# Optimization experiments

Measured on AMD Instinct MI355X. Metric: run time of the kernel, lower is better.

## Reference

```python
import jax, jax.numpy as jnp
import numpy as np

WINDOW = 512  # sliding-window size (keys per query, including self)


def setup_inputs() -> dict:
    key = jax.random.key(0)
    ks = jax.random.split(key, 5)
    B, T, C = 2, 8192, 1024
    s = 1.0 / np.sqrt(C)
    return {
        "x": jax.random.normal(ks[0], (B, T, C), dtype=jnp.float32),
        "Wq": jax.random.normal(ks[1], (C, C), dtype=jnp.float32) * s,
        "Wk": jax.random.normal(ks[2], (C, C), dtype=jnp.float32) * s,
        "Wv": jax.random.normal(ks[3], (C, C), dtype=jnp.float32) * s,
        "Wo": jax.random.normal(ks[4], (C, C), dtype=jnp.float32) * s,
    }


def _block_local_attn(q, k, v, window):
    # q,k,v: [B,H,T,D]; causal sliding-window attention, honoring sparsity by
    # attending only to the current and previous block of size `window`.
    B, H, T, D = q.shape
    W = window
    nb = T // W
    scale = 1.0 / jnp.sqrt(jnp.asarray(D, q.dtype))
    qb = q.reshape(B, H, nb, W, D)
    kb = k.reshape(B, H, nb, W, D)
    vb = v.reshape(B, H, nb, W, D)
    # previous block (zero-padded for block 0)
    kp = jnp.pad(kb, ((0, 0), (0, 0), (1, 0), (0, 0), (0, 0)))[:, :, :nb]
    vp = jnp.pad(vb, ((0, 0), (0, 0), (1, 0), (0, 0), (0, 0)))[:, :, :nb]
    k2 = jnp.concatenate([kp, kb], axis=3)  # [B,H,nb,2W,D]
    v2 = jnp.concatenate([vp, vb], axis=3)
    i = jnp.arange(W)[:, None]          # query index within block
    j = jnp.arange(2 * W)[None, :]      # key index (0..W-1 prev, W..2W-1 cur)
    # key global offset = j - W relative to query block start; causal window of
    # size W (self + W-1 previous) <=> i < j <= i + W
    base = (j > i) & (j <= i + W)                                  # [W,2W]
    prev_ok = (jnp.arange(nb)[:, None] > 0) | (jnp.arange(2 * W)[None, :] >= W)
    mask = base[None, :, :] & prev_ok[:, None, :]                  # [nb,W,2W]
    scores = jnp.einsum("bhnqd,bhnkd->bhnqk", qb, k2) * scale
    scores = jnp.where(mask[None, None], scores, jnp.asarray(-1e30, scores.dtype))
    p = jax.nn.softmax(scores, axis=-1)
    out = jnp.einsum("bhnqk,bhnkd->bhnqd", p, v2)
    return out.reshape(B, H, T, D)


def reference(x, Wq, Wk, Wv, Wo):
    B, T, C = x.shape
    H = 16
    D = C // H
    # nn.Linear(y = x @ W^T), bias=False
    q = (x @ Wq.T).reshape(B, T, H, D).transpose(0, 2, 1, 3)
    k = (x @ Wk.T).reshape(B, T, H, D).transpose(0, 2, 1, 3)
    v = (x @ Wv.T).reshape(B, T, H, D).transpose(0, 2, 1, 3)
    out = _block_local_attn(q, k, v, WINDOW)
    out = out.transpose(0, 2, 1, 3).reshape(B, T, C)
    return out @ Wo.T
```

## Files before the change

kernel.cpp:

```cpp
#include <hip/hip_runtime.h>
#include <hip/hip_bf16.h>
#include <stdint.h>

typedef __attribute__((ext_vector_type(8))) short short8;
typedef __attribute__((ext_vector_type(4))) float f32x4;
typedef __hip_bfloat16 bf16;

#define AS1 __attribute__((address_space(1)))
#define AS3 __attribute__((address_space(3)))

__device__ __forceinline__ void gl16(const void* g, void* l) {
  __builtin_amdgcn_global_load_lds((const AS1 unsigned int*)g,
                                   (AS3 unsigned int*)l, 16, 0, 0);
}

__device__ __forceinline__ unsigned short bfbits(float x) {
  union { bf16 b; unsigned short u; } c; c.b = __float2bfloat16(x); return c.u;
}

#define SCHED0 __builtin_amdgcn_sched_barrier(0)

__global__ __launch_bounds__(256) void k_cvt(const float* __restrict__ src,
                                             bf16* __restrict__ dst, int n8) {
  int i = blockIdx.x * blockDim.x + threadIdx.x;
  int stride = gridDim.x * blockDim.x;
  for (; i < n8; i += stride) {
    const float4* p = (const float4*)src + (size_t)i * 2;
    float4 a = p[0], b = p[1];
    bf16 tmp[8];
    tmp[0] = __float2bfloat16(a.x); tmp[1] = __float2bfloat16(a.y);
    tmp[2] = __float2bfloat16(a.z); tmp[3] = __float2bfloat16(a.w);
    tmp[4] = __float2bfloat16(b.x); tmp[5] = __float2bfloat16(b.y);
    tmp[6] = __float2bfloat16(b.z); tmp[7] = __float2bfloat16(b.w);
    *(short8*)(dst + (size_t)i * 8) = *(short8*)tmp;
  }
}


#define GEMM_BODY(...)                                                         \
  const int Kd = 1024;                                                         \
  const int nk = 32;                                              \
  __shared__ bf16 As[4][256 * 32];                                             \
  __shared__ bf16 Bs[4][256 * 32];                                             \
  int tid = threadIdx.x;                                                       \
  int lane = tid & 63, wid = tid >> 6;                                         \
  int l15 = lane & 15, hi = lane >> 4;                                         \
  int wm = wid >> 2, wn = wid & 3;                                             \
  f32x4 acc[8][4];                                                             \
  _Pragma("unroll") for (int i = 0; i < 8; i++)                                \
      _Pragma("unroll") for (int j = 0; j < 4; j++)                            \
          acc[i][j] = (f32x4){0.f, 0.f, 0.f, 0.f};                             \
  auto stageA = [&](int slot, int kk) {                                        \
    const bf16* ab = Abase + kk * 32;                                          \
    _Pragma("unroll") for (int pass = 0; pass < 2; pass++) {                   \
      int p = pass * 512 + tid;                                                \
      int row = p >> 2;                                                        \
      int u = (p & 3) ^ ((row >> 1) & 3);                                      \
      gl16(ab + (size_t)row * Kd + u * 8, (char*)(&As[slot][0]) + p * 16);     \
    }                                                                          \
  };                                                                           \
  auto stageB = [&](int slot, int kk) {                                        \
    const bf16* bb = Bbase + kk * 32;                                          \
    _Pragma("unroll") for (int pass = 0; pass < 2; pass++) {                   \
      int p = pass * 512 + tid;                                                \
      int row = p >> 2;                                                        \
      int u = (p & 3) ^ ((row >> 1) & 3);                                      \
      gl16(bb + (size_t)row * Kd + u * 8, (char*)(&Bs[slot][0]) + p * 16);     \
    }                                                                          \
  };                                                                           \
  stageA(0, 0); stageB(0, 0);                                                  \
  stageA(1, 1); stageB(1, 1);                                                  \
  stageA(2, 2); stageB(2, 2);                                                  \
  asm volatile("s_waitcnt vmcnt(8)" ::: "memory");                             \
  SCHED0; __builtin_amdgcn_s_barrier(); SCHED0;                                \
  int sw = ((l15 >> 1) & 3) << 4;                                              \
  int arow0 = wm * 128 + l15;                                                  \
  int brow0 = wn * 64 + l15;                                                   \
  short8 a_cur[4], a_hi[4], b_cur[4], b_nxt[4];                                \
  _Pragma("unroll") for (int mf = 0; mf < 4; mf++)                             \
      a_cur[mf] = *(const short8*)((const char*)(&As[0][0]) +                  \
                                   (((arow0 + mf * 16) * 64 + hi * 16) ^ sw)); \
  _Pragma("unroll") for (int nf = 0; nf < 4; nf++)                             \
      b_cur[nf] = *(const short8*)((const char*)(&Bs[0][0]) +                  \
                                   (((brow0 + nf * 16) * 64 + hi * 16) ^ sw)); \
  _Pragma("unroll 2") for (int t = 0; t < nk; ++t) {                           \
    int slot = t & 3;                                                          \
    const char* Ab = (const char*)(&As[slot][0]);                              \
             \
    if (t + 3 < nk) stageA((t + 3) & 3, t + 3);                                \
    _Pragma("unroll") for (int mf = 0; mf < 4; mf++)                           \
        a_hi[mf] = *(const short8*)(Ab +                                       \
            (((arow0 + 64 + mf * 16) * 64 + hi * 16) ^ sw));                   \
    SCHED0;                                                                    \
    __builtin_amdgcn_s_setprio(1);                                             \
    _Pragma("unroll") for (int mf = 0; mf < 4; mf++)                           \
        _Pragma("unroll") for (int nf = 0; nf < 4; nf++)                       \
            acc[mf][nf] = __builtin_amdgcn_mfma_f32_16x16x32_bf16(             \
                a_cur[mf], b_cur[nf], acc[mf][nf], 0, 0, 0);                   \
    __builtin_amdgcn_s_setprio(0);                                             \
    SCHED0;                                                                    \
      \
    if (t + 3 < nk) stageB((t + 3) & 3, t + 3);                                \
    if (t + 1 < nk) {                                                          \
      SCHED0;                                                                  \
      if (t + 3 < nk)      asm volatile("s_waitcnt vmcnt(8)" ::: "memory");    \
      else if (t + 2 < nk) asm volatile("s_waitcnt vmcnt(4)" ::: "memory");    \
      else                 asm volatile("s_waitcnt vmcnt(0)" ::: "memory");    \
      SCHED0; __builtin_amdgcn_s_barrier(); SCHED0;                            \
      const char* AbN = (const char*)(&As[(t + 1) & 3][0]);                    \
      const char* BbN = (const char*)(&Bs[(t + 1) & 3][0]);                    \
      _Pragma("unroll") for (int mf = 0; mf < 4; mf++)                         \
          a_cur[mf] = *(const short8*)(AbN +                                   \
              (((arow0 + mf * 16) * 64 + hi * 16) ^ sw));                      \
      _Pragma("unroll") for (int nf = 0; nf < 4; nf++)                         \
          b_nxt[nf] = *(const short8*)(BbN +                                   \
              (((brow0 + nf * 16) * 64 + hi * 16) ^ sw));                      \
      SCHED0;                                                                  \
    }                                                                          \
    __builtin_amdgcn_s_setprio(1);                                             \
    _Pragma("unroll") for (int mf = 0; mf < 4; mf++)                           \
        _Pragma("unroll") for (int nf = 0; nf < 4; nf++)                       \
            acc[mf + 4][nf] = __builtin_amdgcn_mfma_f32_16x16x32_bf16(         \
                a_hi[mf], b_cur[nf], acc[mf + 4][nf], 0, 0, 0);                \
    __builtin_amdgcn_s_setprio(0);                                             \
    SCHED0;                                                                    \
    if (t + 1 < nk) { __builtin_amdgcn_s_barrier(); SCHED0; }                  \
    _Pragma("unroll") for (int nf = 0; nf < 4; nf++) b_cur[nf] = b_nxt[nf];    \
  }                                                                            \
  __VA_ARGS__

__global__ __launch_bounds__(512, 2) void k_qkv_gemm(
    const bf16* __restrict__ X, const bf16* __restrict__ Wq,
    const bf16* __restrict__ Wk, const bf16* __restrict__ Wv,
    bf16* __restrict__ Q, bf16* __restrict__ K, bf16* __restrict__ V) {
  int bid = blockIdx.x;
  int wsel = bid >> 8;
  int rem = bid & 255;
  int mt = rem & 63;
  int nt = rem >> 6;
  const bf16* W = (wsel == 0) ? Wq : (wsel == 1) ? Wk : Wv;
  bf16* Dst = (wsel == 0) ? Q : (wsel == 1) ? K : V;
  const bf16* Abase = X + (size_t)mt * 256 * 1024;
  const bf16* Bbase = W + (size_t)nt * 256 * 1024;
  GEMM_BODY({
    _Pragma("unroll") for (int mf = 0; mf < 8; mf++) {
      _Pragma("unroll") for (int r = 0; r < 4; r++) {
        int row = mt * 256 + wm * 128 + mf * 16 + hi * 4 + r;
        int b = row >> 13;
        int tok = row & 8191;
        _Pragma("unroll") for (int nf = 0; nf < 4; nf++) {
          int col = nt * 256 + wn * 64 + nf * 16 + l15;
          int h = col >> 6;
          int d = col & 63;
          Dst[((size_t)(b * 16 + h) * 8192 + tok) * 64 + d] =
              __float2bfloat16(acc[mf][nf][r]);
        }
      }
    }
  })
}

__global__ __launch_bounds__(512, 2) void k_out_gemm(
    const bf16* __restrict__ A, const bf16* __restrict__ Wo,
    float* __restrict__ Out) {
  int bid = blockIdx.x;
  int mt = bid & 63;
  int nt = bid >> 6;
  const bf16* Abase = A + (size_t)mt * 256 * 1024;
  const bf16* Bbase = Wo + (size_t)nt * 256 * 1024;
  GEMM_BODY({
    _Pragma("unroll") for (int mf = 0; mf < 8; mf++) {
      _Pragma("unroll") for (int r = 0; r < 4; r++) {
        int row = mt * 256 + wm * 128 + mf * 16 + hi * 4 + r;
        _Pragma("unroll") for (int nf = 0; nf < 4; nf++) {
          int col = nt * 256 + wn * 64 + nf * 16 + l15;
          Out[(size_t)row * 1024 + col] = acc[mf][nf][r];
        }
      }
    }
  })
}

__global__ __launch_bounds__(256) void k_vtrans(const bf16* __restrict__ V,
                                                bf16* __restrict__ VT) {
  const int T = 8192;
  __shared__ bf16 tile[64][72];
  int bid = blockIdx.x;
  int tb = bid & 127;
  int bh = bid >> 7;
  int t0 = tb * 64;
  int tid = threadIdx.x;
  int r = tid >> 2, c4 = tid & 3;
  const bf16* src = V + ((size_t)bh * T + t0 + r) * 64 + c4 * 16;
  short8 a = *(const short8*)src;
  short8 b2 = *(const short8*)(src + 8);
#pragma unroll
  for (int e = 0; e < 8; e++) tile[r][c4 * 16 + e] = ((bf16*)&a)[e];
#pragma unroll
  for (int e = 0; e < 8; e++) tile[r][c4 * 16 + 8 + e] = ((bf16*)&b2)[e];
  __syncthreads();
  alignas(16) bf16 o[16];
#pragma unroll
  for (int e = 0; e < 16; e++) o[e] = tile[c4 * 16 + e][r];
  bf16* dst = VT + ((size_t)bh * 64 + r) * T + t0 + c4 * 16;
  *(short8*)dst = *(short8*)o;
  *(short8*)(dst + 8) = *((short8*)o + 1);
}

__global__ __launch_bounds__(256) void k_attn(
    const bf16* __restrict__ Q, const bf16* __restrict__ K,
    const bf16* __restrict__ VT, bf16* __restrict__ ATT) {
  const int T = 8192;
  __shared__ bf16 Ks[2][64 * 64];
  __shared__ bf16 Vs[2][64 * 64];
  __shared__ bf16 Ps[4][16 * 64];
  int bid = blockIdx.x;
  int qt = bid & 127;
  int bh = bid >> 7;
  int b = bh >> 4, h = bh & 15;
  int tid = threadIdx.x;
  int lane = tid & 63, wid = tid >> 6;
  int l15 = lane & 15, hi = lane >> 4;
  int q0 = qt * 64;
  int qw = q0 + wid * 16;

  short8 bq[2];
  const bf16* qp = Q + ((size_t)bh * T + qw + l15) * 64 + hi * 8;
  bq[0] = *(const short8*)qp;
  bq[1] = *(const short8*)(qp + 32);

  const bf16* Kbh = K + (size_t)bh * T * 64;
  const bf16* Vbh = VT + (size_t)bh * 64 * T;

  auto stage = [&](int bb, int c0) {
#pragma unroll
    for (int pass = 0; pass < 2; pass++) {
      int p = pass * 256 + tid;
      int row = p >> 3;
      int u = (p & 7) ^ (row & 7);
      gl16(Kbh + ((size_t)(c0 + row)) * 64 + u * 8, (char*)(&Ks[bb][0]) + p * 16);
      gl16(Vbh + (size_t)row * T + c0 + u * 8, (char*)(&Vs[bb][0]) + p * 16);
    }
  };

  int cstart = q0 - 512; if (cstart < 0) cstart = 0;
  int nch = (q0 + 64 - cstart) >> 6;

  f32x4 oacc[4];
#pragma unroll
  for (int c = 0; c < 4; c++) oacc[c] = (f32x4){0.f, 0.f, 0.f, 0.f};
  float m = -1e30f, ssum = 0.f;

  stage(0, cstart);
  __syncthreads();
  int buf = 0;
  for (int ci = 0; ci < nch; ci++) {
    int c0 = cstart + (ci << 6);
    if (ci + 1 < nch) stage(buf ^ 1, c0 + 64);
    f32x4 sacc[4];
#pragma unroll
    for (int ks = 0; ks < 4; ks++) sacc[ks] = (f32x4){0.f, 0.f, 0.f, 0.f};
#pragma unroll
    for (int dh = 0; dh < 2; dh++) {
#pragma unroll
      for (int ks = 0; ks < 4; ks++) {
        int krow = ks * 16 + l15;
        int boff = ((krow * 64 + dh * 32 + hi * 8) * 2) ^ ((krow & 7) << 4);
        short8 ak = *(const short8*)((const char*)(&Ks[buf][0]) + boff);
        sacc[ks] = __builtin_amdgcn_mfma_f32_16x16x32_bf16(ak, bq[dh], sacc[ks], 0, 0, 0);
      }
    }
    int qg = qw + l15;
    float pv[4][4];
    float pmax = -1e30f;
#pragma unroll
    for (int ks = 0; ks < 4; ks++)
#pragma unroll
      for (int r = 0; r < 4; r++) {
        int jg = c0 + ks * 16 + hi * 4 + r;
        float s = sacc[ks][r] * 0.125f;
        bool ok = (jg <= qg) && (jg > qg - 512);
        s = ok ? s : -1e30f;
        pv[ks][r] = s;
        pmax = fmaxf(pmax, s);
      }
    pmax = fmaxf(pmax, __shfl_xor(pmax, 16));
    pmax = fmaxf(pmax, __shfl_xor(pmax, 32));
    float mnew = fmaxf(m, pmax);
    float corr = __expf(m - mnew);
    float psum = 0.f;
#pragma unroll
    for (int ks = 0; ks < 4; ks++)
#pragma unroll
      for (int r = 0; r < 4; r++) {
        float p = (pv[ks][r] > -1e29f) ? __expf(pv[ks][r] - mnew) : 0.f;
        pv[ks][r] = p;
        psum += p;
      }
    psum += __shfl_xor(psum, 16);
    psum += __shfl_xor(psum, 32);
    ssum = ssum * corr + psum;
    m = mnew;
#pragma unroll
    for (int r = 0; r < 4; r++) {
      float f = __shfl(corr, hi * 4 + r);
#pragma unroll
      for (int c = 0; c < 4; c++) oacc[c][r] *= f;
    }
#pragma unroll
    for (int ks = 0; ks < 4; ks++) {
      unsigned int lo = (unsigned)bfbits(pv[ks][0]) | ((unsigned)bfbits(pv[ks][1]) << 16);
      unsigned int hi2 = (unsigned)bfbits(pv[ks][2]) | ((unsigned)bfbits(pv[ks][3]) << 16);
      int j0 = ks * 16 + hi * 4;
      int a0 = ((l15 * 64 + j0) * 2) ^ ((l15 & 7) << 4);
      int a1 = ((l15 * 64 + j0 + 2) * 2) ^ ((l15 & 7) << 4);
      *(unsigned int*)((char*)(&Ps[wid][0]) + a0) = lo;
      *(unsigned int*)((char*)(&Ps[wid][0]) + a1) = hi2;
    }
    short8 ap[2];
#pragma unroll
    for (int js = 0; js < 2; js++) {
      int a = ((l15 * 64 + js * 32 + hi * 8) * 2) ^ ((l15 & 7) << 4);
      ap[js] = *(const short8*)((const char*)(&Ps[wid][0]) + a);
    }
#pragma unroll
    for (int js = 0; js < 2; js++)
#pragma unroll
      for (int c = 0; c < 4; c++) {
        int vrow = c * 16 + l15;
        int boff = ((vrow * 64 + js * 32 + hi * 8) * 2) ^ ((vrow & 7) << 4);
        short8 bv = *(const short8*)((const char*)(&Vs[buf][0]) + boff);
        oacc[c] = __builtin_amdgcn_mfma_f32_16x16x32_bf16(ap[js], bv, oacc[c], 0, 0, 0);
      }
    __syncthreads();
    buf ^= 1;
  }
  float inv = 1.f / ssum;
#pragma unroll
  for (int r = 0; r < 4; r++) {
    float f = __shfl(inv, hi * 4 + r);
    int tok = qw + hi * 4 + r;
    bf16* dst = ATT + ((size_t)b * 8192 + tok) * 1024 + h * 64;
#pragma unroll
    for (int c = 0; c < 4; c++)
      dst[c * 16 + l15] = __float2bfloat16(oacc[c][r] * f);
  }
}

extern "C" void kernel_launch(void* const* d_in, const int* in_sizes, int n_in,
                              void* d_out, int out_size, void* d_ws, size_t ws_size,
                              hipStream_t stream) {
  const float* x  = (const float*)d_in[0];
  const float* wq = (const float*)d_in[1];
  const float* wk = (const float*)d_in[2];
  const float* wv = (const float*)d_in[3];
  const float* wo = (const float*)d_in[4];
  float* out = (float*)d_out;

  char* ws = (char*)d_ws;
  const size_t SZ_X = (size_t)16384 * 1024 * 2;
  const size_t SZ_W = (size_t)1024 * 1024 * 2;
  size_t off = 0;
  bf16* xb  = (bf16*)(ws + off); off += SZ_X;
  bf16* wqb = (bf16*)(ws + off); off += SZ_W;
  bf16* wkb = (bf16*)(ws + off); off += SZ_W;
  bf16* wvb = (bf16*)(ws + off); off += SZ_W;
  bf16* wob = (bf16*)(ws + off); off += SZ_W;
  bf16* qb  = (bf16*)(ws + off); off += SZ_X;
  bf16* kb  = (bf16*)(ws + off); off += SZ_X;
  bf16* vb  = (bf16*)(ws + off); off += SZ_X;
  bf16* vtb = (bf16*)(ws + off); off += SZ_X;
  bf16* att = xb;

  k_cvt<<<2048, 256, 0, stream>>>(x, xb, 16384 * 1024 / 8);
  k_cvt<<<512, 256, 0, stream>>>(wq, wqb, 1024 * 1024 / 8);
  k_cvt<<<512, 256, 0, stream>>>(wk, wkb, 1024 * 1024 / 8);
  k_cvt<<<512, 256, 0, stream>>>(wv, wvb, 1024 * 1024 / 8);
  k_cvt<<<512, 256, 0, stream>>>(wo, wob, 1024 * 1024 / 8);
  k_qkv_gemm<<<768, 512, 0, stream>>>(xb, wqb, wkb, wvb, qb, kb, vb);
  k_vtrans<<<4096, 256, 0, stream>>>(vb, vtb);
  k_attn<<<4096, 256, 0, stream>>>(qb, kb, vtb, att);
  k_out_gemm<<<256, 512, 0, stream>>>(att, wob, out);
}
```

Measured before the change: 310.4 us.

## Enlarge attention query tile, remap GEMM block order, and double-buffer A fragments

The attention kernel now handles 128 queries per block with 8 waves instead of 64 with 4, so each staged K/V chunk feeds twice as many queries. This cuts redundant K/V loads across the overlapping windows. Both GEMMs remap block indices so that neighbouring workgroups share operand tiles, aiming for better L2 locality. The GEMM main loop also prefetches the next A fragment into registers, loads the upper A half earlier, and issues stageB after the barrier with a changed vmcnt wait. This raises register pressure, and some masked chunk work rises for the larger query tile.

```diff
diff --git a/kernel.cpp b/kernel.cpp
--- a/kernel.cpp
+++ b/kernel.cpp
@@ -74,58 +74,61 @@
   asm volatile("s_waitcnt vmcnt(8)" ::: "memory");                             \
   SCHED0; __builtin_amdgcn_s_barrier(); SCHED0;                                \
   int sw = ((l15 >> 1) & 3) << 4;                                              \
-  int arow0 = wm * 128 + l15;                                                  \
-  int brow0 = wn * 64 + l15;                                                   \
-  short8 a_cur[4], a_hi[4], b_cur[4], b_nxt[4];                                \
+  int arow = wm * 128 + l15;                                                   \
+  int brow = wn * 64 + l15;                                                    \
+  short8 ax[4], ahi[4], bcur[4], axn[4], bn[4];                                \
   _Pragma("unroll") for (int mf = 0; mf < 4; mf++)                             \
-      a_cur[mf] = *(const short8*)((const char*)(&As[0][0]) +                  \
-                                   (((arow0 + mf * 16) * 64 + hi * 16) ^ sw)); \
+      ax[mf] = *(const short8*)((const char*)(&As[0][0]) +                     \
+                                (((arow + mf * 16) * 64 + hi * 16) ^ sw));     \
   _Pragma("unroll") for (int nf = 0; nf < 4; nf++)                             \
-      b_cur[nf] = *(const short8*)((const char*)(&Bs[0][0]) +                  \
-                                   (((brow0 + nf * 16) * 64 + hi * 16) ^ sw)); \
+      bcur[nf] = *(const short8*)((const char*)(&Bs[0][0]) +                   \
+                                  (((brow + nf * 16) * 64 + hi * 16) ^ sw));   \
   _Pragma("unroll 2") for (int t = 0; t < nk; ++t) {                           \
-    int slot = t & 3;                                                          \
-    const char* Ab = (const char*)(&As[slot][0]);                              \
-             \
+    int s = t & 3, sn = (t + 1) & 3;                                           \
+    const char* Ab = (const char*)(&As[s][0]);                                 \
+          \
+    _Pragma("unroll") for (int mf = 0; mf < 4; mf++)                           \
+        ahi[mf] = *(const short8*)(Ab +                                        \
+            (((arow + 64 + mf * 16) * 64 + hi * 16) ^ sw));                    \
     if (t + 3 < nk) stageA((t + 3) & 3, t + 3);                                \
-    _Pragma("unroll") for (int mf = 0; mf < 4; mf++)                           \
-        a_hi[mf] = *(const short8*)(Ab +                                       \
-            (((arow0 + 64 + mf * 16) * 64 + hi * 16) ^ sw));                   \
     SCHED0;                                                                    \
     __builtin_amdgcn_s_setprio(1);                                             \
     _Pragma("unroll") for (int mf = 0; mf < 4; mf++)                           \
         _Pragma("unroll") for (int nf = 0; nf < 4; nf++)                       \
             acc[mf][nf] = __builtin_amdgcn_mfma_f32_16x16x32_bf16(             \
-                a_cur[mf], b_cur[nf], acc[mf][nf], 0, 0, 0);                   \
+                ax[mf], bcur[nf], acc[mf][nf], 0, 0, 0);                       \
     __builtin_amdgcn_s_setprio(0);                                             \
     SCHED0;                                                                    \
-      \
-    if (t + 3 < nk) stageB((t + 3) & 3, t + 3);                                \
+         \
     if (t + 1 < nk) {                                                          \
-      SCHED0;                                                                  \
-      if (t + 3 < nk)      asm volatile("s_waitcnt vmcnt(8)" ::: "memory");    \
+      if (t + 3 < nk)      asm volatile("s_waitcnt vmcnt(6)" ::: "memory");    \
       else if (t + 2 < nk) asm volatile("s_waitcnt vmcnt(4)" ::: "memory");    \
       else                 asm volatile("s_waitcnt vmcnt(0)" ::: "memory");    \
       SCHED0; __builtin_amdgcn_s_barrier(); SCHED0;                            \
-      const char* AbN = (const char*)(&As[(t + 1) & 3][0]);                    \
-      const char* BbN = (const char*)(&Bs[(t + 1) & 3][0]);                    \
+      if (t + 3 < nk) stageB((t + 3) & 3, t + 3);                              \
+      const char* AbN = (const char*)(&As[sn][0]);                             \
+      const char* BbN = (const char*)(&Bs[sn][0]);                             \
       _Pragma("unroll") for (int mf = 0; mf < 4; mf++)                         \
-          a_cur[mf] = *(const short8*)(AbN +                                   \
-              (((arow0 + mf * 16) * 64 + hi * 16) ^ sw));                      \
+          axn[mf] = *(const short8*)(AbN +                                     \
+              (((arow + mf * 16) * 64 + hi * 16) ^ sw));                       \
       _Pragma("unroll") for (int nf = 0; nf < 4; nf++)                         \
-          b_nxt[nf] = *(const short8*)(BbN +                                   \
-              (((brow0 + nf * 16) * 64 + hi * 16) ^ sw));                      \
+          bn[nf] = *(const short8*)(BbN +                                      \
+              (((brow + nf * 16) * 64 + hi * 16) ^ sw));                       \
       SCHED0;                                                                  \
     }                                                                          \
     __builtin_amdgcn_s_setprio(1);                                             \
     _Pragma("unroll") for (int mf = 0; mf < 4; mf++)                           \
         _Pragma("unroll") for (int nf = 0; nf < 4; nf++)                       \
             acc[mf + 4][nf] = __builtin_amdgcn_mfma_f32_16x16x32_bf16(         \
-                a_hi[mf], b_cur[nf], acc[mf + 4][nf], 0, 0, 0);                \
+                ahi[mf], bcur[nf], acc[mf + 4][nf], 0, 0, 0);                  \
     __builtin_amdgcn_s_setprio(0);                                             \
     SCHED0;                                                                    \
-    if (t + 1 < nk) { __builtin_amdgcn_s_barrier(); SCHED0; }                  \
-    _Pragma("unroll") for (int nf = 0; nf < 4; nf++) b_cur[nf] = b_nxt[nf];    \
+    if (t + 1 < nk) {                                                          \
+      __builtin_amdgcn_s_barrier(); SCHED0;                                    \
+      _Pragma("unroll") for (int i = 0; i < 4; i++) {                          \
+        ax[i] = axn[i]; bcur[i] = bn[i];                                       \
+      }                                                                        \
+    }                                                                          \
   }                                                                            \
   __VA_ARGS__
 
@@ -136,6 +139,7 @@
   int bid = blockIdx.x;
   int wsel = bid >> 8;
   int rem = bid & 255;
+  rem = (rem & 7) * 32 + (rem >> 3);
   int mt = rem & 63;
   int nt = rem >> 6;
   const bf16* W = (wsel == 0) ? Wq : (wsel == 1) ? Wk : Wv;
@@ -164,6 +168,7 @@
     const bf16* __restrict__ A, const bf16* __restrict__ Wo,
     float* __restrict__ Out) {
   int bid = blockIdx.x;
+  bid = (bid & 7) * 32 + (bid >> 3);
   int mt = bid & 63;
   int nt = bid >> 6;
   const bf16* Abase = A + (size_t)mt * 256 * 1024;
@@ -207,21 +212,21 @@
   *(short8*)(dst + 8) = *((short8*)o + 1);
 }
 
-__global__ __launch_bounds__(256) void k_attn(
+__global__ __launch_bounds__(512) void k_attn(
     const bf16* __restrict__ Q, const bf16* __restrict__ K,
     const bf16* __restrict__ VT, bf16* __restrict__ ATT) {
   const int T = 8192;
   __shared__ bf16 Ks[2][64 * 64];
   __shared__ bf16 Vs[2][64 * 64];
-  __shared__ bf16 Ps[4][16 * 64];
+  __shared__ bf16 Ps[8][16 * 64];
   int bid = blockIdx.x;
-  int qt = bid & 127;
-  int bh = bid >> 7;
+  int qt = bid & 63;
+  int bh = bid >> 6;
   int b = bh >> 4, h = bh & 15;
   int tid = threadIdx.x;
   int lane = tid & 63, wid = tid >> 6;
   int l15 = lane & 15, hi = lane >> 4;
-  int q0 = qt * 64;
+  int q0 = qt * 128;
   int qw = q0 + wid * 16;
 
   short8 bq[2];
@@ -233,18 +238,15 @@
   const bf16* Vbh = VT + (size_t)bh * 64 * T;
 
   auto stage = [&](int bb, int c0) {
-#pragma unroll
-    for (int pass = 0; pass < 2; pass++) {
-      int p = pass * 256 + tid;
-      int row = p >> 3;
-      int u = (p & 7) ^ (row & 7);
-      gl16(Kbh + ((size_t)(c0 + row)) * 64 + u * 8, (char*)(&Ks[bb][0]) + p * 16);
-      gl16(Vbh + (size_t)row * T + c0 + u * 8, (char*)(&Vs[bb][0]) + p * 16);
-    }
+    int p = tid;
+    int row = p >> 3;
+    int u = (p & 7) ^ (row & 7);
+    gl16(Kbh + ((size_t)(c0 + row)) * 64 + u * 8, (char*)(&Ks[bb][0]) + p * 16);
+    gl16(Vbh + (size_t)row * T + c0 + u * 8, (char*)(&Vs[bb][0]) + p * 16);
   };
 
   int cstart = q0 - 512; if (cstart < 0) cstart = 0;
-  int nch = (q0 + 64 - cstart) >> 6;
+  int nch = (q0 + 128 - cstart) >> 6;
 
   f32x4 oacc[4];
 #pragma unroll
@@ -379,6 +381,6 @@
   k_cvt<<<512, 256, 0, stream>>>(wo, wob, 1024 * 1024 / 8);
   k_qkv_gemm<<<768, 512, 0, stream>>>(xb, wqb, wkb, wvb, qb, kb, vb);
   k_vtrans<<<4096, 256, 0, stream>>>(vb, vtb);
-  k_attn<<<4096, 256, 0, stream>>>(qb, kb, vtb, att);
+  k_attn<<<2048, 512, 0, stream>>>(qb, kb, vtb, att);
   k_out_gemm<<<256, 512, 0, stream>>>(att, wob, out);
 }
```

New measurement: 348.5 us. 12.3% more time.
